# Optimization experiments

Hardware: AMD Instinct MI355X
Metric: run time of the kernel (lower is better)

Reference implementation:

```python
import jax, jax.numpy as jnp
import numpy as np

BLOCK_SIZE = 256
N_EMBD = 256
HEAD_SIZE = 64


def setup_inputs() -> dict:
    key = jax.random.key(0)
    k1, k2, k3, k4, k5 = jax.random.split(key, 5)
    B, T = 256, 256
    x = jax.random.normal(k1, (B, T, N_EMBD), dtype=jnp.float32)
    # nn.Linear(n_embd, head_size, bias=False) weights, stored as [in, out] for x @ W
    s = 1.0 / np.sqrt(N_EMBD)
    Wk = jax.random.uniform(k2, (N_EMBD, HEAD_SIZE), minval=-s, maxval=s, dtype=jnp.float32)
    Wq = jax.random.uniform(k3, (N_EMBD, HEAD_SIZE), minval=-s, maxval=s, dtype=jnp.float32)
    Wv = jax.random.uniform(k4, (N_EMBD, HEAD_SIZE), minval=-s, maxval=s, dtype=jnp.float32)
    rel_pos_embedding = 0.02 * jax.random.normal(k5, (2 * BLOCK_SIZE - 1, HEAD_SIZE), dtype=jnp.float32)
    return {"x": x, "Wk": Wk, "Wq": Wq, "Wv": Wv, "rel_pos_embedding": rel_pos_embedding}


def reference(x, Wk, Wq, Wv, rel_pos_embedding):
    B, T, C = x.shape
    H = Wk.shape[-1]
    k = x @ Wk  # [B,T,H]
    q = x @ Wq  # [B,T,H]
    v = x @ Wv  # [B,T,H]
    # content scores (scaled); note: position scores are NOT scaled, matching original
    content = jnp.einsum('bth,bsh->bts', q, k) * (H ** -0.5)  # [B,T,T]
    # relative position indices: j - i + (block_size - 1)
    idx = jnp.arange(T)[None, :] - jnp.arange(T)[:, None] + (BLOCK_SIZE - 1)  # [T,T]
    rel_emb = rel_pos_embedding[idx]  # [T,T,H]
    position = jnp.einsum('bth,tsh->bts', q, rel_emb)  # [B,T,T]
    wei = content + position
    causal = jnp.tril(jnp.ones((T, T), dtype=bool))
    wei = jnp.where(causal[None, :, :], wei, -jnp.inf)
    wei = jax.nn.softmax(wei, axis=-1)
    # dropout omitted (eval mode / deterministic reference)
    out = jnp.einsum('bts,bsh->bth', wei, v)  # [B,T,H]
    return out
```

## Files before the change

kernel.cpp:

```cpp
#include <hip/hip_runtime.h>

#define BB 256
#define TT 256
#define CC 256
#define HH 64

typedef _Float16 half8 __attribute__((ext_vector_type(8)));
typedef _Float16 half4 __attribute__((ext_vector_type(4)));
typedef __fp16 fp16x2 __attribute__((ext_vector_type(2)));
typedef float floatx4 __attribute__((ext_vector_type(4)));

__global__ __launch_bounds__(256) void prep(
    const float* __restrict__ rpe,
    const float* __restrict__ Wk, const float* __restrict__ Wq, const float* __restrict__ Wv,
    _Float16* __restrict__ rpeh, _Float16* __restrict__ WT)
{
    const int bid = blockIdx.x, tid = threadIdx.x;
    if (bid < 64) {
        const int i = bid * 256 + tid;
        rpeh[i] = (_Float16)rpe[i];
    } else {
        const int wsel = (bid - 64) >> 6;
        const int n    = (bid - 64) & 63;
        const float* W = wsel == 0 ? Wk : (wsel == 1 ? Wq : Wv);
        WT[(size_t)(wsel * 64 + n) * 256 + tid] = (_Float16)W[tid * HH + n];
    }
}

__device__ __forceinline__ int slot_width(int t) {
    const int j = t >> 1;
    return (j < 2) ? 72 : (32 * j + 40);
}
__device__ __forceinline__ int slot_off(int t) {
    const int j = t >> 1;
    const int V = (j < 2) ? 72 : (32 * j + 40);
    const int S = (j == 0) ? 0 : (j == 1) ? 72 : (16 * j * j + 24 * j + 32);
    return 32 * S + (t & 1) * 16 * V;
}

__global__ __launch_bounds__(1024, 4) void fused(
    const float* __restrict__ x, const _Float16* __restrict__ WT,
    const _Float16* __restrict__ rpeh, float* __restrict__ out)
{
    __shared__ _Float16 lds[75264];
    __shared__ float rowsumP[2][256];
    _Float16* Klds = lds;
    _Float16* VT   = lds + 18432;
    _Float16* pool = lds + 35328;

    const int tid  = threadIdx.x;
    const int b    = blockIdx.x;
    const int w    = tid >> 6;
    const int lane = tid & 63;
    const int quad = lane >> 4;
    const int l    = lane & 15;

    union H8 { half8 v; fp16x2 p[4]; };
    const float4* xg = reinterpret_cast<const float4*>(x);
    const int row0g = b * 256 + w * 16;

    floatx4 acc[12];
#pragma unroll
    for (int nt = 0; nt < 12; ++nt) acc[nt] = (floatx4){0.f, 0.f, 0.f, 0.f};

#pragma unroll
    for (int c = 0; c < 2; ++c) {
#pragma unroll
        for (int i = 0; i < 3; ++i) {
            const int gi  = tid + i * 1024;
            const int row = gi >> 4;
            const int g   = gi & 15;
            *(half8*)&pool[row * 136 + g * 8] =
                *(const half8*)(WT + (size_t)row * 256 + c * 128 + g * 8);
        }
        __syncthreads();

        float4 xa[4][2];
#pragma unroll
        for (int kk = 0; kk < 4; ++kk) {
            const size_t base = (size_t)(row0g + l) * 64 + c * 32 + kk * 8 + quad * 2;
            xa[kk][0] = xg[base];
            xa[kk][1] = xg[base + 1];
        }
#pragma unroll
        for (int kk = 0; kk < 4; ++kk) {
            H8 u;
            u.p[0] = __builtin_amdgcn_cvt_pkrtz(xa[kk][0].x, xa[kk][0].y);
            u.p[1] = __builtin_amdgcn_cvt_pkrtz(xa[kk][0].z, xa[kk][0].w);
            u.p[2] = __builtin_amdgcn_cvt_pkrtz(xa[kk][1].x, xa[kk][1].y);
            u.p[3] = __builtin_amdgcn_cvt_pkrtz(xa[kk][1].z, xa[kk][1].w);
#pragma unroll
            for (int nt = 0; nt < 12; ++nt) {
                const half8 bf = *(const half8*)&pool[(nt * 16 + l) * 136 + kk * 32 + quad * 8];
                acc[nt] = __builtin_amdgcn_mfma_f32_16x16x32_f16(u.v, bf, acc[nt], 0, 0, 0);
            }
        }
        __syncthreads();
    }

    {
        const int trw = w * 16;
#pragma unroll
        for (int nt = 0; nt < 4; ++nt) {
#pragma unroll
            for (int r = 0; r < 4; ++r)
                Klds[(trw + quad * 4 + r) * 72 + nt * 16 + l] = (_Float16)(acc[nt][r] * 0.125f);
            half4 vv;
            vv[0] = (_Float16)acc[nt + 8][0];
            vv[1] = (_Float16)acc[nt + 8][1];
            vv[2] = (_Float16)acc[nt + 8][2];
            vv[3] = (_Float16)acc[nt + 8][3];
            *(half4*)&VT[(nt * 16 + l) * 264 + trw + quad * 4] = vv;
        }
    }
    if (tid < 512) ((float*)rowsumP)[tid] = 0.f;
    __syncthreads();

    _Float16* wh = pool + slot_off(w);
    const int Vw = slot_width(w);
#pragma unroll
    for (int nt = 0; nt < 4; ++nt)
#pragma unroll
        for (int r = 0; r < 4; ++r)
            wh[(quad * 4 + r) * Vw + nt * 16 + l] = (_Float16)acc[nt + 4][r];
    __syncthreads();

    const half8 qf0 = *(const half8*)&wh[l * Vw + quad * 8];
    const half8 qf1 = *(const half8*)&wh[l * Vw + 32 + quad * 8];
    const int tp = 15 - w;
    _Float16* whp = pool + slot_off(tp);
    const int Vp = slot_width(tp);
    half8 qg0 = qf0, qg1 = qf1;
    if (w < 8) {
        qg0 = *(const half8*)&whp[l * Vp + quad * 8];
        qg1 = *(const half8*)&whp[l * Vp + 32 + quad * 8];
    }
    __syncthreads();

    const int jmaxo = (w < 8) ? w : 8;
#pragma unroll
    for (int j = 0; j < 9; ++j) {
        if (j <= jmaxo) {
            const int dt = j + 15 - w;
            const _Float16* rp = rpeh + (size_t)(dt * 16 + l) * HH + quad * 8;
            const half8 bf0 = *(const half8*)rp;
            const half8 bf1 = *(const half8*)(rp + 32);
            floatx4 z = {0.f, 0.f, 0.f, 0.f};
            z = __builtin_amdgcn_mfma_f32_16x16x32_f16(qf0, bf0, z, 0, 0, 0);
            const floatx4 pacc = __builtin_amdgcn_mfma_f32_16x16x32_f16(qf1, bf1, z, 0, 0, 0);
            if (j == 0) {
#pragma unroll
                for (int r = 0; r < 4; ++r) {
                    const int row = quad * 4 + r;
                    const int s   = l + row - 15;
                    if (s >= 0) wh[row * Vw + s] = (_Float16)pacc[r];
                }
            } else {
#pragma unroll
                for (int r = 0; r < 4; ++r) {
                    const int row = quad * 4 + r;
                    wh[row * Vw + 16 * j + l + row - 15] = (_Float16)pacc[r];
                }
            }
        }
    }
    if (w < 8) {
#pragma unroll
        for (int j = 9; j < 16; ++j) {
            if (j <= 15 - w) {
                const int dt = j + w;
                const _Float16* rp = rpeh + (size_t)(dt * 16 + l) * HH + quad * 8;
                const half8 bf0 = *(const half8*)rp;
                const half8 bf1 = *(const half8*)(rp + 32);
                floatx4 z = {0.f, 0.f, 0.f, 0.f};
                z = __builtin_amdgcn_mfma_f32_16x16x32_f16(qg0, bf0, z, 0, 0, 0);
                const floatx4 pacc = __builtin_amdgcn_mfma_f32_16x16x32_f16(qg1, bf1, z, 0, 0, 0);
#pragma unroll
                for (int r = 0; r < 4; ++r) {
                    const int row = quad * 4 + r;
                    whp[row * Vp + 16 * j + l + row - 15] = (_Float16)pacc[r];
                }
            }
        }
    }
    __syncthreads();

    {
        float sumsA[4] = {0.f, 0.f, 0.f, 0.f};
#pragma unroll
        for (int st = 0; st < 9; ++st) {
            if (st <= jmaxo) {
                const _Float16* kp = &Klds[(st * 16 + l) * 72 + quad * 8];
                const half8 kf0 = *(const half8*)kp;
                const half8 kf1 = *(const half8*)(kp + 32);
                floatx4 z = {0.f, 0.f, 0.f, 0.f};
                z = __builtin_amdgcn_mfma_f32_16x16x32_f16(qf0, kf0, z, 0, 0, 0);
                const floatx4 sacc = __builtin_amdgcn_mfma_f32_16x16x32_f16(qf1, kf1, z, 0, 0, 0);
                const int s = l + 16 * st;
                if (st == w) {
#pragma unroll
                    for (int r = 0; r < 4; ++r) {
                        const int row = quad * 4 + r;
                        float e = 0.f;
                        if (l <= row) e = __expf(sacc[r] + (float)wh[row * Vw + s]);
                        sumsA[r] += e;
                        wh[row * Vw + s] = (_Float16)e;
                    }
                    if ((w & 1) == 0) {
                        const int s2 = l + 16 * (st + 1);
#pragma unroll
                        for (int r = 0; r < 4; ++r) wh[(quad * 4 + r) * Vw + s2] = (_Float16)0.f;
                    }
                } else {
#pragma unroll
                    for (int r = 0; r < 4; ++r) {
                        const int row = quad * 4 + r;
                        const float e = __expf(sacc[r] + (float)wh[row * Vw + s]);
                        sumsA[r] += e;
                        wh[row * Vw + s] = (_Float16)e;
                    }
                }
            }
        }
#pragma unroll
        for (int r = 0; r < 4; ++r) {
            float sv = sumsA[r];
            sv += __shfl_xor(sv, 1);
            sv += __shfl_xor(sv, 2);
            sv += __shfl_xor(sv, 4);
            sv += __shfl_xor(sv, 8);
            if (l == 0) rowsumP[0][16 * w + quad * 4 + r] = sv;
        }
    }
    if (w < 8) {
        float sumsB[4] = {0.f, 0.f, 0.f, 0.f};
#pragma unroll
        for (int st = 9; st < 16; ++st) {
            if (st <= 15 - w) {
                const _Float16* kp = &Klds[(st * 16 + l) * 72 + quad * 8];
                const half8 kf0 = *(const half8*)kp;
                const half8 kf1 = *(const half8*)(kp + 32);
                floatx4 z = {0.f, 0.f, 0.f, 0.f};
                z = __builtin_amdgcn_mfma_f32_16x16x32_f16(qg0, kf0, z, 0, 0, 0);
                const floatx4 sacc = __builtin_amdgcn_mfma_f32_16x16x32_f16(qg1, kf1, z, 0, 0, 0);
                const int s = l + 16 * st;
                if (st == tp) {
#pragma unroll
                    for (int r = 0; r < 4; ++r) {
                        const int row = quad * 4 + r;
                        float e = 0.f;
                        if (l <= row) e = __expf(sacc[r] + (float)whp[row * Vp + s]);
                        sumsB[r] += e;
                        whp[row * Vp + s] = (_Float16)e;
                    }
                    if ((tp & 1) == 0) {
                        const int s2 = l + 16 * (st + 1);
#pragma unroll
                        for (int r = 0; r < 4; ++r) whp[(quad * 4 + r) * Vp + s2] = (_Float16)0.f;
                    }
                } else {
#pragma unroll
                    for (int r = 0; r < 4; ++r) {
                        const int row = quad * 4 + r;
                        const float e = __expf(sacc[r] + (float)whp[row * Vp + s]);
                        sumsB[r] += e;
                        whp[row * Vp + s] = (_Float16)e;
                    }
                }
            }
        }
#pragma unroll
        for (int r = 0; r < 4; ++r) {
            float sv = sumsB[r];
            sv += __shfl_xor(sv, 1);
            sv += __shfl_xor(sv, 2);
            sv += __shfl_xor(sv, 4);
            sv += __shfl_xor(sv, 8);
            if (l == 0) rowsumP[1][16 * tp + quad * 4 + r] = sv;
        }
    }
    __syncthreads();

    {
        const int t1 = w >> 1;
        const int hb = (w & 1) << 1;
#pragma unroll
        for (int sel = 0; sel < 2; ++sel) {
            const int tt = sel ? (15 - t1) : t1;
            const _Float16* ws = pool + slot_off(tt);
            const int Vt    = slot_width(tt);
            const int cmaxt = tt >> 1;
            float inv[4];
#pragma unroll
            for (int r = 0; r < 4; ++r) {
                const int row = 16 * tt + quad * 4 + r;
                inv[r] = 1.0f / (rowsumP[0][row] + rowsumP[1][row]);
            }
            floatx4 o0 = {0.f, 0.f, 0.f, 0.f};
            floatx4 o1 = {0.f, 0.f, 0.f, 0.f};
#pragma unroll
            for (int c = 0; c < 8; ++c) {
                if (c <= cmaxt) {
                    const half8 af  = *(const half8*)&ws[l * Vt + c * 32 + quad * 8];
                    const half8 vf0 = *(const half8*)&VT[((hb + 0) * 16 + l) * 264 + c * 32 + quad * 8];
                    const half8 vf1 = *(const half8*)&VT[((hb + 1) * 16 + l) * 264 + c * 32 + quad * 8];
                    o0 = __builtin_amdgcn_mfma_f32_16x16x32_f16(af, vf0, o0, 0, 0, 0);
                    o1 = __builtin_amdgcn_mfma_f32_16x16x32_f16(af, vf1, o1, 0, 0, 0);
                }
            }
#pragma unroll
            for (int r = 0; r < 4; ++r) {
                const int t = 16 * tt + quad * 4 + r;
                out[(size_t)(b * TT + t) * HH + (hb + 0) * 16 + l] = o0[r] * inv[r];
                out[(size_t)(b * TT + t) * HH + (hb + 1) * 16 + l] = o1[r] * inv[r];
            }
        }
    }
}

extern "C" void kernel_launch(void* const* d_in, const int* in_sizes, int n_in,
                              void* d_out, int out_size, void* d_ws, size_t ws_size,
                              hipStream_t stream) {
    const float* x   = (const float*)d_in[0];
    const float* Wk  = (const float*)d_in[1];
    const float* Wq  = (const float*)d_in[2];
    const float* Wv  = (const float*)d_in[3];
    const float* rpe = (const float*)d_in[4];
    float* out = (float*)d_out;

    _Float16* rpeh = (_Float16*)d_ws;
    _Float16* WT   = rpeh + 256 * HH;

    prep<<<dim3(256), dim3(256), 0, stream>>>(rpe, Wk, Wq, Wv, rpeh, WT);
    fused<<<dim3(BB), dim3(1024), 0, stream>>>(x, WT, rpeh, out);
}
```

Before: 123.5 us.

## Switch QKV projection to 32x32x16 MFMA with 2D wave tiling

The QKV projection changes from 16-row waves running 12 16x16x32 MFMAs each to a 2D split: 8 row blocks of 32 rows times 2 column halves, with each wave running three 32x32x16 MFMAs. This lowers LDS B-operand reads per MFMA and the instruction count. The x loads are issued before the barrier so they overlap the weight staging. Q is now written straight into the per-wave slots in the epilogue, which removes one store pass and one __syncthreads.

```diff
diff --git a/kernel.cpp b/kernel.cpp
--- a/kernel.cpp
+++ b/kernel.cpp
@@ -9,6 +9,7 @@
 typedef _Float16 half4 __attribute__((ext_vector_type(4)));
 typedef __fp16 fp16x2 __attribute__((ext_vector_type(2)));
 typedef float floatx4 __attribute__((ext_vector_type(4)));
+typedef float floatx16 __attribute__((ext_vector_type(16)));
 
 __global__ __launch_bounds__(256) void prep(
     const float* __restrict__ rpe,
@@ -54,16 +55,21 @@
     const int lane = tid & 63;
     const int quad = lane >> 4;
     const int l    = lane & 15;
+    const int r32  = lane & 31;
+    const int l5   = lane >> 5;
+    const int rb   = w & 7;
+    const int ch   = w >> 3;
 
     union H8 { half8 v; fp16x2 p[4]; };
     const float4* xg = reinterpret_cast<const float4*>(x);
-    const int row0g = b * 256 + w * 16;
-
-    floatx4 acc[12];
-#pragma unroll
-    for (int nt = 0; nt < 12; ++nt) acc[nt] = (floatx4){0.f, 0.f, 0.f, 0.f};
-
-#pragma unroll
+    const size_t xrow = (size_t)(b * 256 + rb * 32 + r32) * 64;
+
+    floatx16 acc[3];
+#pragma unroll
+    for (int j = 0; j < 3; ++j)
+#pragma unroll
+        for (int e = 0; e < 16; ++e) acc[j][e] = 0.f;
+
     for (int c = 0; c < 2; ++c) {
 #pragma unroll
         for (int i = 0; i < 3; ++i) {
@@ -73,44 +79,65 @@
             *(half8*)&pool[row * 136 + g * 8] =
                 *(const half8*)(WT + (size_t)row * 256 + c * 128 + g * 8);
         }
+        float4 xa[4][2];
+#pragma unroll
+        for (int s = 0; s < 4; ++s) {
+            const size_t base = xrow + c * 32 + s * 4 + l5 * 2;
+            xa[s][0] = xg[base];
+            xa[s][1] = xg[base + 1];
+        }
         __syncthreads();
 
-        float4 xa[4][2];
-#pragma unroll
-        for (int kk = 0; kk < 4; ++kk) {
-            const size_t base = (size_t)(row0g + l) * 64 + c * 32 + kk * 8 + quad * 2;
-            xa[kk][0] = xg[base];
-            xa[kk][1] = xg[base + 1];
-        }
-#pragma unroll
-        for (int kk = 0; kk < 4; ++kk) {
-            H8 u;
-            u.p[0] = __builtin_amdgcn_cvt_pkrtz(xa[kk][0].x, xa[kk][0].y);
-            u.p[1] = __builtin_amdgcn_cvt_pkrtz(xa[kk][0].z, xa[kk][0].w);
-            u.p[2] = __builtin_amdgcn_cvt_pkrtz(xa[kk][1].x, xa[kk][1].y);
-            u.p[3] = __builtin_amdgcn_cvt_pkrtz(xa[kk][1].z, xa[kk][1].w);
-#pragma unroll
-            for (int nt = 0; nt < 12; ++nt) {
-                const half8 bf = *(const half8*)&pool[(nt * 16 + l) * 136 + kk * 32 + quad * 8];
-                acc[nt] = __builtin_amdgcn_mfma_f32_16x16x32_f16(u.v, bf, acc[nt], 0, 0, 0);
+#pragma unroll
+        for (int hb = 0; hb < 2; ++hb) {
+            if (hb == 1) {
+#pragma unroll
+                for (int s = 0; s < 4; ++s) {
+                    const size_t base = xrow + c * 32 + (4 + s) * 4 + l5 * 2;
+                    xa[s][0] = xg[base];
+                    xa[s][1] = xg[base + 1];
+                }
+            }
+#pragma unroll
+            for (int s = 0; s < 4; ++s) {
+                const int ks = hb * 4 + s;
+                H8 u;
+                u.p[0] = __builtin_amdgcn_cvt_pkrtz(xa[s][0].x, xa[s][0].y);
+                u.p[1] = __builtin_amdgcn_cvt_pkrtz(xa[s][0].z, xa[s][0].w);
+                u.p[2] = __builtin_amdgcn_cvt_pkrtz(xa[s][1].x, xa[s][1].y);
+                u.p[3] = __builtin_amdgcn_cvt_pkrtz(xa[s][1].z, xa[s][1].w);
+#pragma unroll
+                for (int j = 0; j < 3; ++j) {
+                    const half8 bf = *(const half8*)&pool[
+                        (size_t)((2 * j + ch) * 32 + r32) * 136 + ks * 16 + l5 * 8];
+                    acc[j] = __builtin_amdgcn_mfma_f32_32x32x16_f16(u.v, bf, acc[j], 0, 0, 0);
+                }
             }
         }
         __syncthreads();
     }
 
     {
-        const int trw = w * 16;
-#pragma unroll
-        for (int nt = 0; nt < 4; ++nt) {
-#pragma unroll
-            for (int r = 0; r < 4; ++r)
-                Klds[(trw + quad * 4 + r) * 72 + nt * 16 + l] = (_Float16)(acc[nt][r] * 0.125f);
+        const int cb = ch * 32;
+        _Float16* sA = pool + slot_off(2 * rb);
+        _Float16* sB = pool + slot_off(2 * rb + 1);
+        const int Vs = slot_width(2 * rb);
+#pragma unroll
+        for (int g = 0; g < 4; ++g) {
+#pragma unroll
+            for (int r = 0; r < 4; ++r) {
+                const int reg = g * 4 + r;
+                const int row = r + 8 * g + 4 * l5;
+                Klds[(rb * 32 + row) * 72 + cb + r32] = (_Float16)(acc[0][reg] * 0.125f);
+                _Float16* qs = (row < 16) ? sA : sB;
+                qs[(row & 15) * Vs + cb + r32] = (_Float16)acc[1][reg];
+            }
             half4 vv;
-            vv[0] = (_Float16)acc[nt + 8][0];
-            vv[1] = (_Float16)acc[nt + 8][1];
-            vv[2] = (_Float16)acc[nt + 8][2];
-            vv[3] = (_Float16)acc[nt + 8][3];
-            *(half4*)&VT[(nt * 16 + l) * 264 + trw + quad * 4] = vv;
+            vv[0] = (_Float16)acc[2][g * 4 + 0];
+            vv[1] = (_Float16)acc[2][g * 4 + 1];
+            vv[2] = (_Float16)acc[2][g * 4 + 2];
+            vv[3] = (_Float16)acc[2][g * 4 + 3];
+            *(half4*)&VT[(size_t)(cb + r32) * 264 + rb * 32 + g * 8 + l5 * 4] = vv;
         }
     }
     if (tid < 512) ((float*)rowsumP)[tid] = 0.f;
@@ -118,12 +145,6 @@
 
     _Float16* wh = pool + slot_off(w);
     const int Vw = slot_width(w);
-#pragma unroll
-    for (int nt = 0; nt < 4; ++nt)
-#pragma unroll
-        for (int r = 0; r < 4; ++r)
-            wh[(quad * 4 + r) * Vw + nt * 16 + l] = (_Float16)acc[nt + 4][r];
-    __syncthreads();
 
     const half8 qf0 = *(const half8*)&wh[l * Vw + quad * 8];
     const half8 qf1 = *(const half8*)&wh[l * Vw + 32 + quad * 8];
```

Measured after the change: 131.5 us. 6.4% more time.
